# Kernel optimization log

Measured on AMD Instinct MI355X. Metric: run time of the kernel, lower is better.

Reference implementation:

```python
import jax, jax.numpy as jnp
import numpy as np

NEG_SLOPE_ATT = 0.2   # GATConv internal leaky_relu slope
NEG_SLOPE_ACT = 0.01  # f.leaky_relu default
LN_EPS = 1e-5

N_NODES, N_EDGES, F_IN = 50000, 400000, 256
HEADS, C1, C2, N_CLS = 4, 256, 128, 32


def gat_conv(x, src, dst, W, a_src, a_dst, bias, concat):
    """PyG GATConv (self-loops already appended to src/dst)."""
    N = x.shape[0]
    H, C = a_src.shape
    h = (x @ W.T).reshape(N, H, C)                      # [N,H,C]
    s = (h * a_src[None]).sum(-1)                       # [N,H] alpha_src
    d = (h * a_dst[None]).sum(-1)                       # [N,H] alpha_dst
    e = jax.nn.leaky_relu(s[src] + d[dst], NEG_SLOPE_ATT)  # [E,H]
    emax = jax.ops.segment_max(e, dst, num_segments=N)
    emax = jnp.where(jnp.isfinite(emax), emax, 0.0)
    p = jnp.exp(e - emax[dst])
    denom = jax.ops.segment_sum(p, dst, num_segments=N)
    alpha = p / (denom[dst] + 1e-16)                    # segment softmax over dst
    out = jax.ops.segment_sum(alpha[:, :, None] * h[src], dst, num_segments=N)
    out = out.reshape(N, H * C) if concat else out.mean(axis=1)
    return out + bias


def layer_norm(x, g, b):
    mu = x.mean(-1, keepdims=True)
    var = jnp.var(x, axis=-1, keepdims=True)
    return (x - mu) / jnp.sqrt(var + LN_EPS) * g + b


def setup_inputs() -> dict:
    key = jax.random.key(0)
    ks = jax.random.split(key, 24)
    def g(k, shape, scale=0.1):
        return jax.random.normal(k, shape, dtype=jnp.float32) * scale
    inp = {
        "x": g(ks[0], (N_NODES, F_IN), 1.0),
        "edge_src": jax.random.randint(ks[1], (N_EDGES,), 0, N_NODES, dtype=jnp.int32),
        "edge_dst": jax.random.randint(ks[2], (N_EDGES,), 0, N_NODES, dtype=jnp.int32),
        # layer 1: in F_IN -> H*C1 (concat)
        "W1": g(ks[3], (HEADS * C1, F_IN)),
        "a_src1": g(ks[4], (HEADS, C1)), "a_dst1": g(ks[5], (HEADS, C1)),
        "b1": jnp.zeros((HEADS * C1,), jnp.float32),
        "ln1_g": jnp.ones((HEADS * C1,), jnp.float32), "ln1_b": jnp.zeros((HEADS * C1,), jnp.float32),
        # layer 2: in H*C1 -> H*C2 (concat)
        "W2": g(ks[6], (HEADS * C2, HEADS * C1)),
        "a_src2": g(ks[7], (HEADS, C2)), "a_dst2": g(ks[8], (HEADS, C2)),
        "b2": jnp.zeros((HEADS * C2,), jnp.float32),
        "ln2_g": jnp.ones((HEADS * C2,), jnp.float32), "ln2_b": jnp.zeros((HEADS * C2,), jnp.float32),
        # layer 3: in H*C2 -> N_CLS (heads=1, mean/no-concat)
        "W3": g(ks[9], (1 * N_CLS, HEADS * C2)),
        "a_src3": g(ks[10], (1, N_CLS)), "a_dst3": g(ks[11], (1, N_CLS)),
        "b3": jnp.zeros((N_CLS,), jnp.float32),
        "ln3_g": jnp.ones((N_CLS,), jnp.float32), "ln3_b": jnp.zeros((N_CLS,), jnp.float32),
    }
    return inp


def reference(x, edge_src, edge_dst,
              W1, a_src1, a_dst1, b1, ln1_g, ln1_b,
              W2, a_src2, a_dst2, b2, ln2_g, ln2_b,
              W3, a_src3, a_dst3, b3, ln3_g, ln3_b):
    N = x.shape[0]
    loops = jnp.arange(N, dtype=edge_src.dtype)  # GATConv add_self_loops=True
    src = jnp.concatenate([edge_src, loops])
    dst = jnp.concatenate([edge_dst, loops])
    # dropout layers are identity in eval mode
    h = gat_conv(x, src, dst, W1, a_src1, a_dst1, b1, True)
    h = jax.nn.leaky_relu(layer_norm(h, ln1_g, ln1_b), NEG_SLOPE_ACT)
    h = gat_conv(h, src, dst, W2, a_src2, a_dst2, b2, True)
    h = jax.nn.leaky_relu(layer_norm(h, ln2_g, ln2_b), NEG_SLOPE_ACT)
    h = gat_conv(h, src, dst, W3, a_src3, a_dst3, b3, False)
    h = layer_norm(h, ln3_g, ln3_b)
    return jax.nn.log_softmax(h, axis=1)
```

## Files before the change

### kernel.cpp

```cpp
#include <hip/hip_runtime.h>
#include <math.h>


#define NEG_ATT 0.2f
#define NEG_ACT 0.01f

typedef __attribute__((ext_vector_type(8))) short bf16x8;
typedef __attribute__((ext_vector_type(8))) unsigned short u16x8;
typedef __attribute__((ext_vector_type(4))) float f32x4;

__device__ __forceinline__ float bf2f(unsigned short u) {
  union { unsigned int i; float f; } c; c.i = ((unsigned int)u) << 16; return c.f;
}
__device__ __forceinline__ unsigned short f2bf(float f) {
  union { float f; unsigned int i; } c; c.f = f;
  unsigned int r = c.i + 0x7FFFu + ((c.i >> 16) & 1u);
  return (unsigned short)(r >> 16);
}

__global__ void cvt4_kernel(const float* __restrict__ i0, unsigned short* o0, int n0,
                            const float* __restrict__ i1, unsigned short* o1, int n1,
                            const float* __restrict__ i2, unsigned short* o2, int n2,
                            const float* __restrict__ i3, unsigned short* o3, int n3) {
  int i = blockIdx.x * 256 + threadIdx.x;
  const float* in; unsigned short* out; int idx;
  if (i < n0) { in = i0; out = o0; idx = i; }
  else if (i < n0 + n1) { in = i1; out = o1; idx = i - n0; }
  else if (i < n0 + n1 + n2) { in = i2; out = o2; idx = i - n0 - n1; }
  else if (i < n0 + n1 + n2 + n3) { in = i3; out = o3; idx = i - n0 - n1 - n2; }
  else return;
  float4 v0 = reinterpret_cast<const float4*>(in)[idx * 2];
  float4 v1 = reinterpret_cast<const float4*>(in)[idx * 2 + 1];
  ushort4 q0 = make_ushort4(f2bf(v0.x), f2bf(v0.y), f2bf(v0.z), f2bf(v0.w));
  ushort4 q1 = make_ushort4(f2bf(v1.x), f2bf(v1.y), f2bf(v1.z), f2bf(v1.w));
  reinterpret_cast<ushort4*>(out)[idx * 2] = q0;
  reinterpret_cast<ushort4*>(out)[idx * 2 + 1] = q1;
}

__global__ __launch_bounds__(256) void qb_kernel(const float* __restrict__ W1,
    const float* __restrict__ as1, const float* __restrict__ ad1,
    unsigned short* __restrict__ Qb) {
  int r = blockIdx.x;
  int k = threadIdx.x;
  if (r >= 8) { Qb[r * 256 + k] = 0; return; }
  int h = r & 3;
  const float* av = (r >> 2) ? ad1 : as1;
  float acc = 0.f;
#pragma unroll 8
  for (int c = 0; c < 256; c++)
    acc += W1[((size_t)(h * 256 + c)) * 256 + k] * av[h * 256 + c];
  Qb[r * 256 + k] = f2bf(acc);
}

__global__ void hist_kernel(const int* __restrict__ edge_dst,
                            int* __restrict__ cnt, int E, int N) {
  int e = blockIdx.x * 256 + threadIdx.x;
  if (e >= E + N) return;
  int dn = (e < E) ? edge_dst[e] : (e - E);
  atomicAdd(&cnt[dn], 1);
}

__global__ __launch_bounds__(256) void scan1_kernel(
    const int* __restrict__ cnt, int* __restrict__ bsum, int N) {
  __shared__ int sd_[256];
  int i = blockIdx.x * 256 + threadIdx.x;
  int v = (i < N) ? cnt[i] : 0;
  sd_[threadIdx.x] = v;
  __syncthreads();
#pragma unroll
  for (int off = 128; off; off >>= 1) {
    if (threadIdx.x < off) sd_[threadIdx.x] += sd_[threadIdx.x + off];
    __syncthreads();
  }
  if (threadIdx.x == 0) bsum[blockIdx.x] = sd_[0];
}

__global__ __launch_bounds__(256) void scan2_kernel(
    const int* __restrict__ bsum, int* __restrict__ boff,
    int* __restrict__ row_ptr, int NB, int N) {
  __shared__ int sd_[256];
  int t = threadIdx.x;
  int v = (t < NB) ? bsum[t] : 0;
  sd_[t] = v;
  __syncthreads();
#pragma unroll
  for (int off = 1; off < 256; off <<= 1) {
    int u = (t >= off) ? sd_[t - off] : 0;
    __syncthreads();
    sd_[t] += u;
    __syncthreads();
  }
  if (t < NB) boff[t] = sd_[t] - v;
  if (t == 255) row_ptr[N] = sd_[255];
}

__global__ __launch_bounds__(256) void scan3_kernel(
    const int* __restrict__ cnt, const int* __restrict__ boff,
    int* __restrict__ row_ptr, int* __restrict__ cur, int N) {
  __shared__ int sd_[256];
  int t = threadIdx.x;
  int i = blockIdx.x * 256 + t;
  int v = (i < N) ? cnt[i] : 0;
  sd_[t] = v;
  __syncthreads();
#pragma unroll
  for (int off = 1; off < 256; off <<= 1) {
    int u = (t >= off) ? sd_[t - off] : 0;
    __syncthreads();
    sd_[t] += u;
    __syncthreads();
  }
  if (i < N) {
    int val = boff[blockIdx.x] + sd_[t] - v;
    row_ptr[i] = val;
    cur[i] = val;
  }
}

__global__ void scatter_kernel(const int* __restrict__ edge_src,
                               const int* __restrict__ edge_dst,
                               int* __restrict__ cur,
                               int* __restrict__ src_sorted, int E, int N) {
  int e = blockIdx.x * 256 + threadIdx.x;
  if (e >= E + N) return;
  int sn, dn;
  if (e < E) { sn = edge_src[e]; dn = edge_dst[e]; }
  else       { sn = dn = e - E; }
  int pos = atomicAdd(&cur[dn], 1);
  src_sorted[pos] = sn;
}

#define GLOBAL_AS __attribute__((address_space(1)))
#define LDS_AS __attribute__((address_space(3)))

__device__ __forceinline__ void gload_lds16(const void* g, void* l) {
  __builtin_amdgcn_global_load_lds((const GLOBAL_AS unsigned int*)g,
                                   (LDS_AS unsigned int*)l, 16, 0, 0);
}

template <int BM, int BN, int WM, int WN, bool F32OUT, bool SDMODE>
__global__ __launch_bounds__(256) void gemm_mfma(
    const unsigned short* __restrict__ A, const unsigned short* __restrict__ B,
    void* __restrict__ Cv, const float* __restrict__ bias,
    int M, int N, int K, int lda, int ldb, int ldc,
    long long aZ, long long bZ, long long cZ, int biasZ,
    float* __restrict__ sOut, float* __restrict__ dOut,
    const float* __restrict__ a_s, const float* __restrict__ a_d, int H) {
  constexpr int BK = 64;
  constexpr int FM = BM / (WM * 16);
  constexpr int FN = BN / (WN * 16);
  const int flat = blockIdx.x + gridDim.x * (blockIdx.y + gridDim.y * blockIdx.z);
  const int nwg = gridDim.x * gridDim.y * gridDim.z;
  const int xcd = flat & 7, slot = flat >> 3;
  const int q = nwg >> 3, r = nwg & 7;
  const int wgid = (xcd < r ? xcd * (q + 1) : r * (q + 1) + (xcd - r) * q) + slot;
  const int nx = gridDim.x;
  const int per_z = nx * gridDim.y;
  const int bz = wgid / per_z;
  const int rem = wgid - bz * per_z;
  const int bmi = rem / nx;
  const int bni = rem - bmi * nx;

  A += (size_t)bz * aZ;
  B += (size_t)bz * bZ;
  const size_t cbase = (size_t)bz * cZ;
  __shared__ unsigned short As[2][BM * BK];
  __shared__ unsigned short Bs[2][BN * BK];
  const int tid = threadIdx.x;
  const int w = tid >> 6, lane = tid & 63;
  const int wm = w / WN, wn = w % WN;
  const int bm = bmi * BM;
  const int bn = bni * BN;
  const int l15 = lane & 15, l4 = lane >> 4;

  f32x4 acc[FM][FN] = {};

  constexpr int CHA = BM * BK / 8;
  constexpr int CHB = BN * BK / 8;

  auto STAGE = [&](int buf, int k0) {
#pragma unroll
    for (int c0 = 0; c0 < CHA; c0 += 256) {
      int c = c0 + tid;
      if (CHA - c0 >= 256 || tid < CHA - c0) {
        int cl = c ^ ((c >> 3) & 7);
        int row = cl >> 3;
        int kk = (cl & 7) * 8;
        int gr = bm + row; if (gr > M - 1) gr = M - 1;
        gload_lds16(A + (size_t)gr * lda + k0 + kk,
                    As[buf] + (size_t)(c0 + (tid & ~63)) * 8);
      }
    }
#pragma unroll
    for (int c0 = 0; c0 < CHB; c0 += 256) {
      int c = c0 + tid;
      if (CHB - c0 >= 256 || tid < CHB - c0) {
        int cl = c ^ ((c >> 3) & 7);
        int row = cl >> 3;
        int kk = (cl & 7) * 8;
        gload_lds16(B + (size_t)(bn + row) * ldb + k0 + kk,
                    Bs[buf] + (size_t)(c0 + (tid & ~63)) * 8);
      }
    }
  };

  STAGE(0, 0);
  __syncthreads();
  int cur = 0;
  for (int k0 = 0; k0 < K; k0 += BK) {
    if (k0 + BK < K) STAGE(cur ^ 1, k0 + BK);
#pragma unroll
    for (int ks = 0; ks < 2; ks++) {
      bf16x8 af[FM], bfr[FN];
#pragma unroll
      for (int i = 0; i < FM; i++) {
        int row = wm * (FM * 16) + i * 16 + l15;
        int byte = row * (BK * 2) + ks * 64 + l4 * 16;
        byte ^= ((byte >> 7) & 7) << 4;
        af[i] = *reinterpret_cast<const bf16x8*>((const char*)As[cur] + byte);
      }
#pragma unroll
      for (int i = 0; i < FN; i++) {
        int row = wn * (FN * 16) + i * 16 + l15;
        int byte = row * (BK * 2) + ks * 64 + l4 * 16;
        byte ^= ((byte >> 7) & 7) << 4;
        bfr[i] = *reinterpret_cast<const bf16x8*>((const char*)Bs[cur] + byte);
      }
#pragma unroll
      for (int i = 0; i < FM; i++)
#pragma unroll
        for (int jn = 0; jn < FN; jn++)
          acc[i][jn] = __builtin_amdgcn_mfma_f32_16x16x32_bf16(
              af[i], bfr[jn], acc[i][jn], 0, 0, 0);
    }
    __syncthreads();
    cur ^= 1;
  }
  if constexpr (SDMODE) {
    float aws[FN], awd[FN];
#pragma unroll
    for (int jn = 0; jn < FN; jn++) {
      int c = wn * (FN * 16) + jn * 16 + l15;
      aws[jn] = a_s[bni * BN + c];
      awd[jn] = a_d[bni * BN + c];
    }
#pragma unroll
    for (int i = 0; i < FM; i++) {
#pragma unroll
      for (int r2 = 0; r2 < 4; r2++) {
        float ps = 0.f, pd = 0.f;
#pragma unroll
        for (int jn = 0; jn < FN; jn++) {
          ps = fmaf(acc[i][jn][r2], aws[jn], ps);
          pd = fmaf(acc[i][jn][r2], awd[jn], pd);
        }
#pragma unroll
        for (int o = 1; o < 16; o <<= 1) {
          ps += __shfl_xor(ps, o);
          pd += __shfl_xor(pd, o);
        }
        if (l15 == 0) {
          int m = bm + wm * (FM * 16) + i * 16 + l4 * 4 + r2;
          if (m < M) {
            atomicAdd(&sOut[(size_t)m * H + bni], ps);
            atomicAdd(&dOut[(size_t)m * H + bni], pd);
          }
        }
      }
    }
  }
#pragma unroll
  for (int i = 0; i < FM; i++) {
#pragma unroll
    for (int jn = 0; jn < FN; jn++) {
      int col = bn + wn * (FN * 16) + jn * 16 + l15;
      float bv = bias ? bias[biasZ * bz + col] : 0.f;
#pragma unroll
      for (int r2 = 0; r2 < 4; r2++) {
        int m = bm + wm * (FM * 16) + i * 16 + l4 * 4 + r2;
        if (m < M) {
          float val = acc[i][jn][r2] + bv;
          if constexpr (F32OUT)
            ((float*)Cv)[cbase + (size_t)m * ldc + col] = val;
          else
            ((unsigned short*)Cv)[cbase + (size_t)m * ldc + col] = f2bf(val);
        }
      }
    }
  }
}

__global__ __launch_bounds__(256) void aggx_kernel(
    const int* __restrict__ row_ptr, const int* __restrict__ src_sorted,
    const float* __restrict__ sd1, const unsigned short* __restrict__ xb,
    unsigned short* __restrict__ y, int N) {
  __shared__ float alds[4][2][64][4];
  int w = threadIdx.x >> 6, lane = threadIdx.x & 63;
  int n = blockIdx.x * 4 + w;
  if (n >= N) return;
  int beg = row_ptr[n], end = row_ptr[n + 1];
  float4 dv = *reinterpret_cast<const float4*>(sd1 + (size_t)n * 16 + 4);

  auto compE = [&](int t, float e[4]) {
    if (t < end) {
      int sj = src_sorted[t];
      float4 sv = *reinterpret_cast<const float4*>(sd1 + (size_t)sj * 16);
      e[0] = sv.x + dv.x; e[1] = sv.y + dv.y;
      e[2] = sv.z + dv.z; e[3] = sv.w + dv.w;
#pragma unroll
      for (int h = 0; h < 4; h++) e[h] = e[h] > 0.f ? e[h] : NEG_ATT * e[h];
    } else {
      e[0] = e[1] = e[2] = e[3] = -1e30f;
    }
  };

  float mx[4] = {-1e30f, -1e30f, -1e30f, -1e30f};
  for (int cb = beg; cb < end; cb += 64) {
    float e[4]; compE(cb + lane, e);
#pragma unroll
    for (int h = 0; h < 4; h++) {
      float m = e[h];
#pragma unroll
      for (int o = 32; o; o >>= 1) m = fmaxf(m, __shfl_xor(m, o));
      mx[h] = fmaxf(mx[h], m);
    }
  }
  float den[4] = {0.f, 0.f, 0.f, 0.f};
  for (int cb = beg; cb < end; cb += 64) {
    float e[4]; compE(cb + lane, e);
#pragma unroll
    for (int h = 0; h < 4; h++) {
      float p = __expf(e[h] - mx[h]);
#pragma unroll
      for (int o = 32; o; o >>= 1) p += __shfl_xor(p, o);
      den[h] += p;
    }
  }
  float ia[4];
#pragma unroll
  for (int h = 0; h < 4; h++) ia[h] = 1.0f / (den[h] + 1e-16f);

  float acc[4][4] = {};
  for (int cb = beg; cb < end; cb += 64) {
    float e[4]; compE(cb + lane, e);
    int pb = ((cb - beg) >> 6) & 1;
    float4 al;
    al.x = __expf(e[0] - mx[0]) * ia[0];
    al.y = __expf(e[1] - mx[1]) * ia[1];
    al.z = __expf(e[2] - mx[2]) * ia[2];
    al.w = __expf(e[3] - mx[3]) * ia[3];
    *reinterpret_cast<float4*>(alds[w][pb][lane]) = al;
    int cd = end - cb; if (cd > 64) cd = 64;
    for (int j = 0; j < cd; j++) {
      float4 a4 = *reinterpret_cast<const float4*>(alds[w][pb][j]);
      int sj = src_sorted[cb + j];
      ushort4 xv = *reinterpret_cast<const ushort4*>(
          xb + (size_t)sj * 256 + lane * 4);
      float x0 = bf2f(xv.x), x1 = bf2f(xv.y), x2 = bf2f(xv.z), x3 = bf2f(xv.w);
      float ar[4] = {a4.x, a4.y, a4.z, a4.w};
#pragma unroll
      for (int h = 0; h < 4; h++) {
        acc[h][0] = fmaf(ar[h], x0, acc[h][0]);
        acc[h][1] = fmaf(ar[h], x1, acc[h][1]);
        acc[h][2] = fmaf(ar[h], x2, acc[h][2]);
        acc[h][3] = fmaf(ar[h], x3, acc[h][3]);
      }
    }
  }
#pragma unroll
  for (int h = 0; h < 4; h++) {
    ushort4 o = make_ushort4(f2bf(acc[h][0]), f2bf(acc[h][1]),
                             f2bf(acc[h][2]), f2bf(acc[h][3]));
    *reinterpret_cast<ushort4*>(y + (size_t)n * 1024 + h * 256 + lane * 4) = o;
  }
}

__global__ __launch_bounds__(256) void agg2m_kernel(
    const int* __restrict__ row_ptr, const int* __restrict__ src_sorted,
    const float* __restrict__ s2, const float* __restrict__ d2,
    const unsigned short* __restrict__ h2, const float* __restrict__ bias,
    const float* __restrict__ ln_g, const float* __restrict__ ln_b,
    unsigned short* __restrict__ outb, int N) {
  __shared__ float alds[4][2][64][4];
  int w = threadIdx.x >> 6, lane = threadIdx.x & 63;
  int n = blockIdx.x * 4 + w;
  if (n >= N) return;
  int beg = row_ptr[n], end = row_ptr[n + 1];
  int head = lane >> 4, c0 = lane * 8;
  float4 dv = *reinterpret_cast<const float4*>(d2 + (size_t)n * 4);

  auto compE = [&](int t, float e[4]) {
    if (t < end) {
      int sj = src_sorted[t];
      float4 sv = *reinterpret_cast<const float4*>(s2 + (size_t)sj * 4);
      e[0] = sv.x + dv.x; e[1] = sv.y + dv.y;
      e[2] = sv.z + dv.z; e[3] = sv.w + dv.w;
#pragma unroll
      for (int h = 0; h < 4; h++) e[h] = e[h] > 0.f ? e[h] : NEG_ATT * e[h];
    } else {
      e[0] = e[1] = e[2] = e[3] = -1e30f;
    }
  };

  float mx[4] = {-1e30f, -1e30f, -1e30f, -1e30f};
  for (int cb = beg; cb < end; cb += 64) {
    float e[4]; compE(cb + lane, e);
#pragma unroll
    for (int h = 0; h < 4; h++) {
      float m = e[h];
#pragma unroll
      for (int o = 32; o; o >>= 1) m = fmaxf(m, __shfl_xor(m, o));
      mx[h] = fmaxf(mx[h], m);
    }
  }
  float den[4] = {0.f, 0.f, 0.f, 0.f};
  for (int cb = beg; cb < end; cb += 64) {
    float e[4]; compE(cb + lane, e);
#pragma unroll
    for (int h = 0; h < 4; h++) {
      float p = __expf(e[h] - mx[h]);
#pragma unroll
      for (int o = 32; o; o >>= 1) p += __shfl_xor(p, o);
      den[h] += p;
    }
  }
  float ia[4];
#pragma unroll
  for (int h = 0; h < 4; h++) ia[h] = 1.0f / (den[h] + 1e-16f);

  float acc[8] = {};
  for (int cb = beg; cb < end; cb += 64) {
    float e[4]; compE(cb + lane, e);
    int pb = ((cb - beg) >> 6) & 1;
    float4 al;
    al.x = __expf(e[0] - mx[0]) * ia[0];
    al.y = __expf(e[1] - mx[1]) * ia[1];
    al.z = __expf(e[2] - mx[2]) * ia[2];
    al.w = __expf(e[3] - mx[3]) * ia[3];
    *reinterpret_cast<float4*>(alds[w][pb][lane]) = al;
    int cd = end - cb; if (cd > 64) cd = 64;
    for (int j = 0; j < cd; j++) {
      float a = alds[w][pb][j][head];
      int sj = src_sorted[cb + j];
      u16x8 xv = *reinterpret_cast<const u16x8*>(h2 + (size_t)sj * 512 + c0);
#pragma unroll
      for (int i = 0; i < 8; i++)
        acc[i] = fmaf(a, bf2f(xv[i]), acc[i]);
    }
  }
  float v[8], s1 = 0.f, sq = 0.f;
#pragma unroll
  for (int i = 0; i < 8; i++) {
    v[i] = acc[i] + bias[c0 + i];
    s1 += v[i]; sq += v[i] * v[i];
  }
#pragma unroll
  for (int o = 32; o; o >>= 1) { s1 += __shfl_xor(s1, o); sq += __shfl_xor(sq, o); }
  float mean = s1 * (1.0f / 512.0f);
  float var = sq * (1.0f / 512.0f) - mean * mean;
  float rstd = rsqrtf(var + 1e-5f);
  u16x8 ov;
#pragma unroll
  for (int i = 0; i < 8; i++) {
    float yv = (v[i] - mean) * rstd * ln_g[c0 + i] + ln_b[c0 + i];
    yv = yv > 0.f ? yv : NEG_ACT * yv;
    ov[i] = f2bf(yv);
  }
  *reinterpret_cast<u16x8*>(outb + (size_t)n * 512 + c0) = ov;
}

__global__ __launch_bounds__(256) void ln1024_kernel(
    const unsigned short* __restrict__ z, const float* __restrict__ ln_g,
    const float* __restrict__ ln_b, unsigned short* __restrict__ outb, int N) {
  int n = blockIdx.x;
  int tid = threadIdx.x;
  int c0 = tid * 4;
  ushort4 zv = *reinterpret_cast<const ushort4*>(z + (size_t)n * 1024 + c0);
  float v[4] = {bf2f(zv.x), bf2f(zv.y), bf2f(zv.z), bf2f(zv.w)};
  float s1 = v[0] + v[1] + v[2] + v[3];
  float sq = v[0]*v[0] + v[1]*v[1] + v[2]*v[2] + v[3]*v[3];
#pragma unroll
  for (int o = 32; o; o >>= 1) { s1 += __shfl_down(s1, o); sq += __shfl_down(sq, o); }
  __shared__ float r1[4], r2[4];
  int wave = tid >> 6, lane = tid & 63;
  if (lane == 0) { r1[wave] = s1; r2[wave] = sq; }
  __syncthreads();
  float t1 = r1[0] + r1[1] + r1[2] + r1[3];
  float t2 = r2[0] + r2[1] + r2[2] + r2[3];
  float mean = t1 * (1.0f / 1024.0f);
  float var = t2 * (1.0f / 1024.0f) - mean * mean;
  float rstd = rsqrtf(var + 1e-5f);
  ushort4 ov;
  float y0 = (v[0] - mean) * rstd * ln_g[c0 + 0] + ln_b[c0 + 0];
  float y1 = (v[1] - mean) * rstd * ln_g[c0 + 1] + ln_b[c0 + 1];
  float y2 = (v[2] - mean) * rstd * ln_g[c0 + 2] + ln_b[c0 + 2];
  float y3 = (v[3] - mean) * rstd * ln_g[c0 + 3] + ln_b[c0 + 3];
  ov.x = f2bf(y0 > 0.f ? y0 : NEG_ACT * y0);
  ov.y = f2bf(y1 > 0.f ? y1 : NEG_ACT * y1);
  ov.z = f2bf(y2 > 0.f ? y2 : NEG_ACT * y2);
  ov.w = f2bf(y3 > 0.f ? y3 : NEG_ACT * y3);
  *reinterpret_cast<ushort4*>(outb + (size_t)n * 1024 + c0) = ov;
}

__global__ void stats_kernel(const int* __restrict__ row_ptr,
    const int* __restrict__ src_sorted, const float* __restrict__ s,
    const float* __restrict__ d, float* __restrict__ p_sorted,
    float* __restrict__ inv_den, int N) {
  int idx = blockIdx.x * blockDim.x + threadIdx.x;
  if (idx >= N) return;
  int n = idx;
  int beg = row_ptr[n], end = row_ptr[n + 1];
  float dn = d[n];
  float mx = -1e30f;
  for (int j = beg; j < end; j++) {
    float v = s[src_sorted[j]] + dn;
    v = v > 0.f ? v : NEG_ATT * v;
    mx = fmaxf(mx, v);
  }
  float den = 0.f;
  for (int j = beg; j < end; j++) {
    float v = s[src_sorted[j]] + dn;
    v = v > 0.f ? v : NEG_ATT * v;
    float p = __expf(v - mx);
    p_sorted[j] = p;
    den += p;
  }
  inv_den[n] = 1.0f / (den + 1e-16f);
}

__global__ __launch_bounds__(256) void final_kernel(
    const int* __restrict__ row_ptr, const int* __restrict__ src_sorted,
    const float* __restrict__ p_sorted, const float* __restrict__ inv_den,
    const unsigned short* __restrict__ h3, const float* __restrict__ b3,
    const float* __restrict__ g3, const float* __restrict__ bb3,
    float* __restrict__ out, int N) {
  int idx = blockIdx.x * 256 + threadIdx.x;
  int n = idx >> 5, c = idx & 31;
  if (n >= N) return;
  int beg = row_ptr[n], end = row_ptr[n + 1];
  float acc = 0.f;
  for (int j = beg; j < end; j++)
    acc = fmaf(p_sorted[j], bf2f(h3[(size_t)src_sorted[j] * 32 + c]), acc);
  float v = acc * inv_den[n] + b3[c];
  float s1 = v, s2 = v * v;
#pragma unroll
  for (int o = 16; o; o >>= 1) { s1 += __shfl_xor(s1, o, 32); s2 += __shfl_xor(s2, o, 32); }
  float mean = s1 * (1.f / 32.f), var = s2 * (1.f / 32.f) - mean * mean;
  float y = (v - mean) * rsqrtf(var + 1e-5f) * g3[c] + bb3[c];
  float mx = y;
#pragma unroll
  for (int o = 16; o; o >>= 1) mx = fmaxf(mx, __shfl_xor(mx, o, 32));
  float ex = __expf(y - mx), se = ex;
#pragma unroll
  for (int o = 16; o; o >>= 1) se += __shfl_xor(se, o, 32);
  out[(size_t)n * 32 + c] = y - mx - __logf(se);
}

extern "C" void kernel_launch(void* const* d_in, const int* in_sizes, int n_in,
                              void* d_out, int out_size, void* d_ws,
                              size_t ws_size, hipStream_t stream) {
  const float* x   = (const float*)d_in[0];
  const int* esrc  = (const int*)d_in[1];
  const int* edst  = (const int*)d_in[2];
  const float* W1  = (const float*)d_in[3];
  const float* as1 = (const float*)d_in[4];
  const float* ad1 = (const float*)d_in[5];
  const float* b1  = (const float*)d_in[6];
  const float* g1  = (const float*)d_in[7];
  const float* bb1 = (const float*)d_in[8];
  const float* W2  = (const float*)d_in[9];
  const float* as2 = (const float*)d_in[10];
  const float* ad2 = (const float*)d_in[11];
  const float* b2  = (const float*)d_in[12];
  const float* g2  = (const float*)d_in[13];
  const float* bb2 = (const float*)d_in[14];
  const float* W3  = (const float*)d_in[15];
  const float* as3 = (const float*)d_in[16];
  const float* ad3 = (const float*)d_in[17];
  const float* b3  = (const float*)d_in[18];
  const float* g3  = (const float*)d_in[19];
  const float* bb3 = (const float*)d_in[20];
  float* out = (float*)d_out;

  const int Nn = in_sizes[0] / 256;
  const int E  = in_sizes[1];
  const int Etot = E + Nn;
  const int NB = (Nn + 255) / 256;

  char* ws = (char*)d_ws;
  size_t off = 0;
  auto alloc = [&](size_t bytes) -> char* {
    char* p = ws + off;
    off += (bytes + 255) & ~(size_t)255;
    return p;
  };
  int* cnt        = (int*)alloc((size_t)(Nn + 1) * 4);
  int* cur        = (int*)alloc((size_t)(Nn + 1) * 4);
  int* row_ptr    = (int*)alloc((size_t)(Nn + 1) * 4);
  int* bsum       = (int*)alloc(256 * 4);
  int* boff       = (int*)alloc(256 * 4);
  int* src_sorted = (int*)alloc((size_t)Etot * 4);
  float* sd1   = (float*)alloc((size_t)Nn * 16 * 4);
  float* sdbuf = (float*)alloc((size_t)Nn * 10 * 4);
  float* s2 = sdbuf;
  float* d2 = sdbuf + (size_t)Nn * 4;
  float* s3 = sdbuf + (size_t)Nn * 8;
  float* d3 = sdbuf + (size_t)Nn * 9;
  float* invd3 = (float*)alloc((size_t)Nn * 4);
  float* p3    = (float*)alloc((size_t)Etot * 4);
  unsigned short* W1b = (unsigned short*)alloc((size_t)1024 * 256 * 2);
  unsigned short* W2b = (unsigned short*)alloc((size_t)512 * 1024 * 2);
  unsigned short* W3b = (unsigned short*)alloc((size_t)32 * 512 * 2);
  unsigned short* Qb  = (unsigned short*)alloc((size_t)16 * 256 * 2);
  unsigned short* h3  = (unsigned short*)alloc((size_t)Nn * 32 * 2);
  unsigned short* regA = (unsigned short*)alloc((size_t)Nn * 1024 * 2);
  unsigned short* regB = (unsigned short*)alloc((size_t)Nn * 1024 * 2);
  unsigned short* y    = regA;
  unsigned short* act1 = regA;
  unsigned short* act2 = regA;
  unsigned short* xb   = regB;
  unsigned short* z1   = regB;
  unsigned short* h2   = regB;

  const int mb = (Nn + 127) / 128;

  {
    int n0 = Nn * 256 / 8, n1 = 1024 * 256 / 8, n2 = 512 * 1024 / 8, n3 = 32 * 512 / 8;
    int tot = n0 + n1 + n2 + n3;
    cvt4_kernel<<<(tot + 255) / 256, 256, 0, stream>>>(
        x, xb, n0, W1, W1b, n1, W2, W2b, n2, W3, W3b, n3);
  }
  qb_kernel<<<16, 256, 0, stream>>>(W1, as1, ad1, Qb);

  hipMemsetAsync(cnt, 0, (size_t)(Nn + 1) * 4, stream);
  hipMemsetAsync(sdbuf, 0, (size_t)Nn * 10 * 4, stream);
  int eb = (Etot + 255) / 256;
  hist_kernel<<<eb, 256, 0, stream>>>(edst, cnt, E, Nn);
  scan1_kernel<<<NB, 256, 0, stream>>>(cnt, bsum, Nn);
  scan2_kernel<<<1, 256, 0, stream>>>(bsum, boff, row_ptr, NB, Nn);
  scan3_kernel<<<NB, 256, 0, stream>>>(cnt, boff, row_ptr, cur, Nn);
  scatter_kernel<<<eb, 256, 0, stream>>>(esrc, edst, cur, src_sorted, E, Nn);

  gemm_mfma<128, 16, 4, 1, true, false><<<dim3(1, mb, 1), 256, 0, stream>>>(
      xb, Qb, sd1, nullptr, Nn, 16, 256, 256, 256, 16, 0, 0, 0, 0,
      nullptr, nullptr, nullptr, nullptr, 0);
  aggx_kernel<<<(Nn + 3) / 4, 256, 0, stream>>>(row_ptr, src_sorted, sd1, xb, y, Nn);
  gemm_mfma<128, 128, 2, 2, false, false><<<dim3(2, mb, 4), 256, 0, stream>>>(
      y, W1b, z1, b1, Nn, 256, 256, 1024, 256, 1024, 256LL, 256LL * 256, 256LL, 256,
      nullptr, nullptr, nullptr, nullptr, 0);
  ln1024_kernel<<<Nn, 256, 0, stream>>>(z1, g1, bb1, act1, Nn);

  gemm_mfma<128, 128, 2, 2, false, true><<<dim3(4, mb, 1), 256, 0, stream>>>(
      act1, W2b, h2, nullptr, Nn, 512, 1024, 1024, 1024, 512, 0, 0, 0, 0,
      s2, d2, as2, ad2, 4);
  agg2m_kernel<<<(Nn + 3) / 4, 256, 0, stream>>>(row_ptr, src_sorted, s2, d2,
                                                 h2, b2, g2, bb2, act2, Nn);

  gemm_mfma<128, 32, 4, 1, false, true><<<dim3(1, mb, 1), 256, 0, stream>>>(
      act2, W3b, h3, nullptr, Nn, 32, 512, 512, 512, 32, 0, 0, 0, 0,
      s3, d3, as3, ad3, 1);
  stats_kernel<<<(Nn + 255) / 256, 256, 0, stream>>>(row_ptr, src_sorted,
                                                     s3, d3, p3, invd3, Nn);
  final_kernel<<<(Nn * 32 + 255) / 256, 256, 0, stream>>>(row_ptr, src_sorted,
      p3, invd3, h3, b3, g3, bb3, out, Nn);
}
```

Measured before the change: 709.4 us.

## Single-buffer GEMM LDS and reduce SD projections in shared memory

```diff
diff --git a/kernel.cpp b/kernel.cpp
--- a/kernel.cpp
+++ b/kernel.cpp
@@ -164,8 +164,8 @@
   A += (size_t)bz * aZ;
   B += (size_t)bz * bZ;
   const size_t cbase = (size_t)bz * cZ;
-  __shared__ unsigned short As[2][BM * BK];
-  __shared__ unsigned short Bs[2][BN * BK];
+  __shared__ unsigned short As[BM * BK];
+  __shared__ unsigned short Bs[BN * BK];
   const int tid = threadIdx.x;
   const int w = tid >> 6, lane = tid & 63;
   const int wm = w / WN, wn = w % WN;
@@ -178,7 +178,7 @@
   constexpr int CHA = BM * BK / 8;
   constexpr int CHB = BN * BK / 8;
 
-  auto STAGE = [&](int buf, int k0) {
+  for (int k0 = 0; k0 < K; k0 += BK) {
 #pragma unroll
     for (int c0 = 0; c0 < CHA; c0 += 256) {
       int c = c0 + tid;
@@ -188,7 +188,7 @@
         int kk = (cl & 7) * 8;
         int gr = bm + row; if (gr > M - 1) gr = M - 1;
         gload_lds16(A + (size_t)gr * lda + k0 + kk,
-                    As[buf] + (size_t)(c0 + (tid & ~63)) * 8);
+                    As + (size_t)(c0 + (tid & ~63)) * 8);
       }
     }
 #pragma unroll
@@ -199,16 +199,10 @@
         int row = cl >> 3;
         int kk = (cl & 7) * 8;
         gload_lds16(B + (size_t)(bn + row) * ldb + k0 + kk,
-                    Bs[buf] + (size_t)(c0 + (tid & ~63)) * 8);
-      }
-    }
-  };
-
-  STAGE(0, 0);
-  __syncthreads();
-  int cur = 0;
-  for (int k0 = 0; k0 < K; k0 += BK) {
-    if (k0 + BK < K) STAGE(cur ^ 1, k0 + BK);
+                    Bs + (size_t)(c0 + (tid & ~63)) * 8);
+      }
+    }
+    __syncthreads();
 #pragma unroll
     for (int ks = 0; ks < 2; ks++) {
       bf16x8 af[FM], bfr[FN];
@@ -217,14 +211,14 @@
         int row = wm * (FM * 16) + i * 16 + l15;
         int byte = row * (BK * 2) + ks * 64 + l4 * 16;
         byte ^= ((byte >> 7) & 7) << 4;
-        af[i] = *reinterpret_cast<const bf16x8*>((const char*)As[cur] + byte);
+        af[i] = *reinterpret_cast<const bf16x8*>((const char*)As + byte);
       }
 #pragma unroll
       for (int i = 0; i < FN; i++) {
         int row = wn * (FN * 16) + i * 16 + l15;
         int byte = row * (BK * 2) + ks * 64 + l4 * 16;
         byte ^= ((byte >> 7) & 7) << 4;
-        bfr[i] = *reinterpret_cast<const bf16x8*>((const char*)Bs[cur] + byte);
+        bfr[i] = *reinterpret_cast<const bf16x8*>((const char*)Bs + byte);
       }
 #pragma unroll
       for (int i = 0; i < FM; i++)
@@ -234,9 +228,9 @@
               af[i], bfr[jn], acc[i][jn], 0, 0, 0);
     }
     __syncthreads();
-    cur ^= 1;
   }
   if constexpr (SDMODE) {
+    __shared__ float sdl[WN][BM][2];
     float aws[FN], awd[FN];
 #pragma unroll
     for (int jn = 0; jn < FN; jn++) {
@@ -260,12 +254,21 @@
           pd += __shfl_xor(pd, o);
         }
         if (l15 == 0) {
-          int m = bm + wm * (FM * 16) + i * 16 + l4 * 4 + r2;
-          if (m < M) {
-            atomicAdd(&sOut[(size_t)m * H + bni], ps);
-            atomicAdd(&dOut[(size_t)m * H + bni], pd);
-          }
+          int rl = wm * (FM * 16) + i * 16 + l4 * 4 + r2;
+          sdl[wn][rl][0] = ps;
+          sdl[wn][rl][1] = pd;
         }
+      }
+    }
+    __syncthreads();
+    if (tid < BM) {
+      int m = bm + tid;
+      if (m < M) {
+        float ss = 0.f, dd = 0.f;
+#pragma unroll
+        for (int j = 0; j < WN; j++) { ss += sdl[j][tid][0]; dd += sdl[j][tid][1]; }
+        sOut[(size_t)m * H + bni] = ss;
+        dOut[(size_t)m * H + bni] = dd;
       }
     }
   }
@@ -601,11 +604,10 @@
   int* boff       = (int*)alloc(256 * 4);
   int* src_sorted = (int*)alloc((size_t)Etot * 4);
   float* sd1   = (float*)alloc((size_t)Nn * 16 * 4);
-  float* sdbuf = (float*)alloc((size_t)Nn * 10 * 4);
-  float* s2 = sdbuf;
-  float* d2 = sdbuf + (size_t)Nn * 4;
-  float* s3 = sdbuf + (size_t)Nn * 8;
-  float* d3 = sdbuf + (size_t)Nn * 9;
+  float* s2    = (float*)alloc((size_t)Nn * 4 * 4);
+  float* d2    = (float*)alloc((size_t)Nn * 4 * 4);
+  float* s3    = (float*)alloc((size_t)Nn * 4);
+  float* d3    = (float*)alloc((size_t)Nn * 4);
   float* invd3 = (float*)alloc((size_t)Nn * 4);
   float* p3    = (float*)alloc((size_t)Etot * 4);
   unsigned short* W1b = (unsigned short*)alloc((size_t)1024 * 256 * 2);
@@ -633,7 +635,6 @@
   qb_kernel<<<16, 256, 0, stream>>>(W1, as1, ad1, Qb);
 
   hipMemsetAsync(cnt, 0, (size_t)(Nn + 1) * 4, stream);
-  hipMemsetAsync(sdbuf, 0, (size_t)Nn * 10 * 4, stream);
   int eb = (Etot + 255) / 256;
   hist_kernel<<<eb, 256, 0, stream>>>(edst, cnt, E, Nn);
   scan1_kernel<<<NB, 256, 0, stream>>>(cnt, bsum, Nn);
```

After: 658.0 us. -7.3%, faster.
